# Kernel optimization log

Hardware: AMD Instinct MI355X
Metric: run time of the kernel (lower is better)

The kernel has to match this reference:

```python
import jax, jax.numpy as jnp
import numpy as np

B, S, T, V, E, H = 32, 64, 64, 32000, 256, 512


def lstm_layer(x, h0, c0, Wih, Whh, bih, bhh):
    """PyTorch-convention LSTM layer. x: [B,T,in]; gates order i,f,g,o."""
    xg = jnp.einsum('bti,gi->btg', x, Wih) + (bih + bhh)  # [B,T,4H] precomputed input gates

    def step(carry, xt):
        h, c = carry
        g = xt + h @ Whh.T
        i, f, gg, o = jnp.split(g, 4, axis=-1)
        c = jax.nn.sigmoid(f) * c + jax.nn.sigmoid(i) * jnp.tanh(gg)
        h = jax.nn.sigmoid(o) * jnp.tanh(c)
        return (h, c), h

    (hT, cT), ys = jax.lax.scan(step, (h0, c0), xg.transpose(1, 0, 2))
    return ys.transpose(1, 0, 2), hT, cT


def setup_inputs() -> dict:
    key = jax.random.key(0)
    ks = jax.random.split(key, 32)
    w = lambda k, shape: jax.random.normal(k, shape, jnp.float32) * 0.05
    return {
        'source': jax.random.randint(ks[0], (B, S), 0, V),
        'target': jax.random.randint(ks[1], (B, T), 0, V),
        'enc_emb': w(ks[2], (V, E)),
        'enc_Wih0': w(ks[3], (4 * H, E)),
        'enc_Whh0': w(ks[4], (4 * H, H)),
        'enc_bih0': w(ks[5], (4 * H,)),
        'enc_bhh0': w(ks[6], (4 * H,)),
        'enc_Wih1': w(ks[7], (4 * H, H)),
        'enc_Whh1': w(ks[8], (4 * H, H)),
        'enc_bih1': w(ks[9], (4 * H,)),
        'enc_bhh1': w(ks[10], (4 * H,)),
        'dec_emb': w(ks[11], (V, E)),
        'dec_Wih0': w(ks[12], (4 * H, E)),
        'dec_Whh0': w(ks[13], (4 * H, H)),
        'dec_bih0': w(ks[14], (4 * H,)),
        'dec_bhh0': w(ks[15], (4 * H,)),
        'dec_Wih1': w(ks[16], (4 * H, H)),
        'dec_Whh1': w(ks[17], (4 * H, H)),
        'dec_bih1': w(ks[18], (4 * H,)),
        'dec_bhh1': w(ks[19], (4 * H,)),
        'aff_W': w(ks[20], (V, H)),
        'aff_b': w(ks[21], (V,)),
    }


def reference(source, target, enc_emb, enc_Wih0, enc_Whh0, enc_bih0, enc_bhh0,
              enc_Wih1, enc_Whh1, enc_bih1, enc_bhh1, dec_emb,
              dec_Wih0, dec_Whh0, dec_bih0, dec_bhh0,
              dec_Wih1, dec_Whh1, dec_bih1, dec_bhh1, aff_W, aff_b):
    b = source.shape[0]
    z = jnp.zeros((b, H), jnp.float32)
    # Encoder: 2-layer LSTM over source, keep final (h,c) per layer
    x = enc_emb[source]                                   # [B,S,E]
    y0, h0, c0 = lstm_layer(x, z, z, enc_Wih0, enc_Whh0, enc_bih0, enc_bhh0)
    _, h1, c1 = lstm_layer(y0, z, z, enc_Wih1, enc_Whh1, enc_bih1, enc_bhh1)
    # Decoder: original loop is always teacher-forced (input = target[:, i]),
    # so it equals one full-sequence LSTM over target[:, :-1].
    dx = dec_emb[target[:, :-1]]                          # [B,T-1,E]
    d0, _, _ = lstm_layer(dx, h0, c0, dec_Wih0, dec_Whh0, dec_bih0, dec_bhh0)
    d1, _, _ = lstm_layer(d0, h1, c1, dec_Wih1, dec_Whh1, dec_bih1, dec_bhh1)
    logits = jnp.einsum('bth,vh->btv', d1, aff_W) + aff_b  # [B,T-1,V]
    # outputs[:,0,:] stays zero as in the original
    return jnp.concatenate([jnp.zeros((b, 1, logits.shape[-1]), logits.dtype), logits], axis=1)
```

## Files before the change

kernel.cpp:

```cpp
#include <hip/hip_runtime.h>
#include <hip/hip_bf16.h>

using bf16 = __hip_bfloat16;
typedef __bf16 bf16x8 __attribute__((ext_vector_type(8)));
typedef float f32x4 __attribute__((ext_vector_type(4)));
typedef int i32x4 __attribute__((ext_vector_type(4)));
typedef short short4v __attribute__((ext_vector_type(4)));
typedef short short8v __attribute__((ext_vector_type(8)));

#define DEV __device__ __forceinline__


DEV unsigned short f2bf(float f) {
  unsigned u = __builtin_bit_cast(unsigned, f);
  u = (u + 0x7fffu + ((u >> 16) & 1u)) >> 16;
  return (unsigned short)u;
}

DEV f32x4 mfma16(bf16x8 a, bf16x8 b, f32x4 c) {
  return __builtin_amdgcn_mfma_f32_16x16x32_bf16(a, b, c, 0, 0, 0);
}

DEV void llc_load16(bf16x8* dst, const bf16* p) {
  i32x4 r;
  asm volatile("global_load_dwordx4 %0, %1, off sc0 sc1" : "=v"(r) : "v"(p) : "memory");
  *dst = __builtin_bit_cast(bf16x8, r);
}
DEV void llc_store16(void* p, short8v v) {
  asm volatile("global_store_dwordx4 %0, %1, off sc0 sc1"
               :: "v"(p), "v"(__builtin_bit_cast(i32x4, v)) : "memory");
}
DEV void llc_store_f32(float* p, float v) {
  asm volatile("global_store_dword %0, %1, off sc0 sc1" :: "v"(p), "v"(v) : "memory");
}
DEV float llc_load_f32(const float* p) {
  float r;
  asm volatile("global_load_dword %0, %1, off sc0 sc1\n\ts_waitcnt vmcnt(0)"
               : "=v"(r) : "v"(p) : "memory");
  return r;
}
DEV void llc_store_flag(unsigned* p, unsigned v) {
  asm volatile("global_store_dword %0, %1, off sc0 sc1" :: "v"(p), "v"(v) : "memory");
}

DEV void poll16(const unsigned* base, int wave, int lane) {
  const unsigned* p = base + (long)(wave * 16 + (lane & 15)) * 32;
  while (true) {
    unsigned v = __hip_atomic_load(p, __ATOMIC_RELAXED, __HIP_MEMORY_SCOPE_SYSTEM);
    if (__all(v != 0u)) break;
    __builtin_amdgcn_s_sleep(1);
  }
}
DEV void poll64(const unsigned* base, int lane) {
  const unsigned* p = base + (long)lane * 32;
  while (true) {
    unsigned v = __hip_atomic_load(p, __ATOMIC_RELAXED, __HIP_MEMORY_SCOPE_SYSTEM);
    if (__all(v != 0u)) break;
    __builtin_amdgcn_s_sleep(1);
  }
}

struct ConvJobs {
  const float* src[9];
  bf16* dst[9];
  int n[9];
  int cnt;
};

__global__ void convert_all(ConvJobs jobs) {
  long base = (long)blockIdx.x * blockDim.x + threadIdx.x;
  long stride = (long)gridDim.x * blockDim.x;
  for (int ji = 0; ji < jobs.cnt; ++ji) {
    const float* s = jobs.src[ji];
    bf16* d = jobs.dst[ji];
    long n4 = (long)jobs.n[ji] >> 2;
    for (long i = base; i < n4; i += stride) {
      f32x4 v = *(const f32x4*)(s + i * 4);
      short4v o;
#pragma unroll
      for (int j = 0; j < 4; ++j) o[j] = (short)f2bf(v[j]);
      *(short4v*)((short*)d + i * 4) = o;
    }
  }
}

__global__ void embed_gather(const int* __restrict__ ids, const float* __restrict__ emb,
                             bf16* __restrict__ out, int rows, int ids_stride) {
  long total = (long)rows * 64;
  long stride = (long)gridDim.x * blockDim.x;
  for (long i = (long)blockIdx.x * blockDim.x + threadIdx.x; i < total; i += stride) {
    int row = (int)(i >> 6);
    int e = ((int)i & 63) * 4;
    int b = row & 31;
    int t = row >> 5;
    int id = ids[b * ids_stride + t];
    f32x4 v = *(const f32x4*)(emb + (long)id * 256 + e);
    short4v o;
#pragma unroll
    for (int j = 0; j < 4; ++j) o[j] = (short)f2bf(v[j]);
    *(short4v*)((short*)out + (long)row * 256 + e) = o;
  }
}

__global__ void zero_t0(float* __restrict__ out) {
  long total = 32l * 8000;
  long stride = (long)gridDim.x * blockDim.x;
  f32x4 z{};
  for (long i = (long)blockIdx.x * blockDim.x + threadIdx.x; i < total; i += stride) {
    long b = i / 8000;
    long v = i - b * 8000;
    *(f32x4*)(out + b * 64 * 32000 + v * 4) = z;
  }
}

__launch_bounds__(256)
__global__ void gemm_bf16(const bf16* __restrict__ A, const void* __restrict__ Wv, int b_fp32,
                          const float* __restrict__ bias1, const float* __restrict__ bias2,
                          float* __restrict__ C, int M, int N, int K, int affine_remap) {
  __shared__ __align__(16) bf16 As[128][64];
  __shared__ __align__(16) bf16 Bs[128][64];
  int nm = (M + 127) >> 7;
  int mt_blk = blockIdx.x % nm;
  int nt_blk = blockIdx.x / nm;
  long m0 = (long)mt_blk * 128, n0 = (long)nt_blk * 128;
  int tid = threadIdx.x;
  int lane = tid & 63, wave = tid >> 6;
  int wm = wave & 1, wn = wave >> 1;
  int fl = lane & 15, fg = lane >> 4;
  const bf16* Wb = (const bf16*)Wv;
  const float* Wf = (const float*)Wv;
  f32x4 acc[4][4] = {};

  for (int k0 = 0; k0 < K; k0 += 64) {
    __syncthreads();
#pragma unroll
    for (int i = 0; i < 4; ++i) {
      int e = (i * 256 + tid) * 8;
      int row = e >> 6;
      int col = e & 63;
      long ar = m0 + row; if (ar >= M) ar = M - 1;
      *(bf16x8*)(&As[row][col]) = *(const bf16x8*)(A + ar * (long)K + k0 + col);
      long br = n0 + row; if (br >= N) br = N - 1;
      if (b_fp32) {
        const float* p = Wf + br * (long)K + k0 + col;
        f32x4 v0 = *(const f32x4*)p;
        f32x4 v1 = *(const f32x4*)(p + 4);
        short8v o;
#pragma unroll
        for (int j = 0; j < 4; ++j) { o[j] = (short)f2bf(v0[j]); o[j + 4] = (short)f2bf(v1[j]); }
        *(short8v*)(&Bs[row][col]) = o;
      } else {
        *(bf16x8*)(&Bs[row][col]) = *(const bf16x8*)(Wb + br * (long)K + k0 + col);
      }
    }
    __syncthreads();
#pragma unroll
    for (int kt = 0; kt < 2; ++kt) {
      bf16x8 af[4], bfr[4];
#pragma unroll
      for (int x = 0; x < 4; ++x)
        af[x] = *(const bf16x8*)(&As[wm * 64 + x * 16 + fl][kt * 32 + fg * 8]);
#pragma unroll
      for (int x = 0; x < 4; ++x)
        bfr[x] = *(const bf16x8*)(&Bs[wn * 64 + x * 16 + fl][kt * 32 + fg * 8]);
#pragma unroll
      for (int mi = 0; mi < 4; ++mi)
#pragma unroll
        for (int ni = 0; ni < 4; ++ni)
          acc[mi][ni] = mfma16(af[mi], bfr[ni], acc[mi][ni]);
    }
  }
#pragma unroll
  for (int mi = 0; mi < 4; ++mi) {
#pragma unroll
    for (int ni = 0; ni < 4; ++ni) {
#pragma unroll
      for (int r = 0; r < 4; ++r) {
        long row = m0 + wm * 64 + mi * 16 + fg * 4 + r;
        long col = n0 + wn * 64 + ni * 16 + fl;
        if (row < M && col < N) {
          float v = acc[mi][ni][r];
          if (bias1) v += bias1[col];
          if (bias2) v += bias2[col];
          long orow = row;
          if (affine_remap) orow = (long)(row & 31) * 64 + (row >> 5) + 1;
          C[orow * (long)N + col] = v;
        }
      }
    }
  }
}

struct FusedParams {
  const bf16* wih[4]; const bf16* whh[4];
  const float* bih[4]; const float* bhh[4];
  const bf16* x[4];
  bf16* y[4];
  const bf16* hinit[4];
  const float* cinit[4];
  float* cfin[4];
  unsigned* flags;
};

DEV unsigned* FL(unsigned* flags, int l, int t) {
  return flags + ((long)(l * 64 + t) * 64) * 32;
}

__launch_bounds__(256)
__global__ void lstm_fused(FusedParams P) {
  __shared__ float part[4][32][33];
  __shared__ __align__(16) unsigned short h_sh[32][8];
  const int tid = threadIdx.x;
  const int lane = tid & 63, wave = tid >> 6;
  const int fl = lane & 15, fg = lane >> 4;
  const int l = blockIdx.x >> 6;
  const int slc = blockIdx.x & 63;
  const int n0 = slc * 8;
  const int b_t = tid & 31, d_t = tid >> 5;
  const int T = (l < 2) ? 64 : 63;
  const int Kx = (l & 1) ? 512 : 256;
  const int xspan = Kx >> 2;
  const int ktx = xspan >> 5;
  const bf16* __restrict__ Wih = P.wih[l];
  const bf16* __restrict__ Whh = P.whh[l];
  const bf16* __restrict__ X = P.x[l];
  bf16* __restrict__ Y = P.y[l];
  const bf16* __restrict__ Hinit = P.hinit[l];
  unsigned* flags = P.flags;

  float bsum[4];
#pragma unroll
  for (int gi = 0; gi < 4; ++gi)
    bsum[gi] = P.bih[l][gi * 512 + n0 + d_t] + P.bhh[l][gi * 512 + n0 + d_t];

  bf16x8 wfx[2][4], wfh[2][4];
#pragma unroll
  for (int nt = 0; nt < 2; ++nt) {
    int j = nt * 16 + fl;
    long row = (long)(j >> 3) * 512 + n0 + (j & 7);
#pragma unroll
    for (int kt = 0; kt < 4; ++kt) {
      if (kt < ktx)
        wfx[nt][kt] =
            *(const bf16x8*)(Wih + row * (long)Kx + wave * xspan + kt * 32 + fg * 8);
      wfh[nt][kt] = *(const bf16x8*)(Whh + row * 512l + wave * 128 + kt * 32 + fg * 8);
    }
  }
  float c = 0.f;

  for (int t = 0; t < T; ++t) {
    const unsigned* fb = (l == 1) ? FL(flags, 0, t) : (l == 3) ? FL(flags, 2, t) : nullptr;
    if (fb) poll16(fb, wave, lane);

    const bf16* xb = X + (long)t * 32 * Kx;
    bf16x8 xa0[4], xa1[4];
#pragma unroll
    for (int kt = 0; kt < 4; ++kt) {
      if (kt < ktx) {
        int k = wave * xspan + kt * 32 + fg * 8;
        const bf16* p0 = xb + (long)fl * Kx + k;
        const bf16* p1 = xb + (long)(fl + 16) * Kx + k;
        if (l & 1) {
          llc_load16(&xa0[kt], p0);
          llc_load16(&xa1[kt], p1);
        } else {
          xa0[kt] = *(const bf16x8*)p0;
          xa1[kt] = *(const bf16x8*)p1;
        }
      }
    }
    asm volatile("s_waitcnt vmcnt(0)" ::: "memory");
    __builtin_amdgcn_sched_barrier(0);
    f32x4 acc[2][2] = {};
#pragma unroll
    for (int kt = 0; kt < 4; ++kt) {
      if (kt < ktx) {
        acc[0][0] = mfma16(xa0[kt], wfx[0][kt], acc[0][0]);
        acc[0][1] = mfma16(xa0[kt], wfx[1][kt], acc[0][1]);
        acc[1][0] = mfma16(xa1[kt], wfx[0][kt], acc[1][0]);
        acc[1][1] = mfma16(xa1[kt], wfx[1][kt], acc[1][1]);
      }
    }

    if (t > 0) poll16(FL(flags, l, t - 1), wave, lane);
    else if (l == 2) poll64(FL(flags, 0, 63), lane);
    else if (l == 3) poll64(FL(flags, 1, 63), lane);
    if (t == 0) c = llc_load_f32(P.cinit[l] + (long)b_t * 512 + n0 + d_t);

    const bf16* hb = (t == 0) ? Hinit : (Y + (long)(t - 1) * 32 * 512);
    bf16x8 ha0[4], ha1[4];
#pragma unroll
    for (int kt = 0; kt < 4; ++kt) {
      int k = wave * 128 + kt * 32 + fg * 8;
      llc_load16(&ha0[kt], hb + (long)fl * 512 + k);
      llc_load16(&ha1[kt], hb + (long)(fl + 16) * 512 + k);
    }
    asm volatile("s_waitcnt vmcnt(0)" ::: "memory");
    __builtin_amdgcn_sched_barrier(0);
#pragma unroll
    for (int kt = 0; kt < 4; ++kt) {
      acc[0][0] = mfma16(ha0[kt], wfh[0][kt], acc[0][0]);
      acc[0][1] = mfma16(ha0[kt], wfh[1][kt], acc[0][1]);
      acc[1][0] = mfma16(ha1[kt], wfh[0][kt], acc[1][0]);
      acc[1][1] = mfma16(ha1[kt], wfh[1][kt], acc[1][1]);
    }
#pragma unroll
    for (int mt = 0; mt < 2; ++mt)
#pragma unroll
      for (int nt = 0; nt < 2; ++nt)
#pragma unroll
        for (int r = 0; r < 4; ++r)
          part[wave][mt * 16 + fg * 4 + r][nt * 16 + fl] = acc[mt][nt][r];
    __syncthreads();

    float g4[4];
#pragma unroll
    for (int gi = 0; gi < 4; ++gi) {
      int j = gi * 8 + d_t;
      g4[gi] = part[0][b_t][j] + part[1][b_t][j] + part[2][b_t][j] + part[3][b_t][j] +
               bsum[gi];
    }
    float ig = 1.f / (1.f + __expf(-g4[0]));
    float ff = 1.f / (1.f + __expf(-g4[1]));
    float gg = tanhf(g4[2]);
    float og = 1.f / (1.f + __expf(-g4[3]));
    c = ff * c + ig * gg;
    float h = og * tanhf(c);
    h_sh[b_t][d_t] = f2bf(h);
    if (t == T - 1) {
      llc_store_f32(P.cfin[l] + (long)b_t * 512 + n0 + d_t, c);
      asm volatile("s_waitcnt vmcnt(0)" ::: "memory");
    }
    __syncthreads();
    if (wave == 0) {
      if (lane < 32)
        llc_store16((unsigned short*)Y + ((long)t * 32 + lane) * 512 + n0,
                    *(const short8v*)(&h_sh[lane][0]));
      asm volatile("s_waitcnt vmcnt(0)" ::: "memory");
      if (lane == 0)
        llc_store_flag(FL(flags, l, t) + (long)slc * 32, 1u);
      asm volatile("s_waitcnt vmcnt(0)" ::: "memory");
    }
  }
}

extern "C" void kernel_launch(void* const* d_in, const int* in_sizes, int n_in,
                              void* d_out, int out_size, void* d_ws, size_t ws_size,
                              hipStream_t stream) {
  (void)in_sizes; (void)n_in; (void)out_size;
  const int*   source   = (const int*)d_in[0];
  const int*   target   = (const int*)d_in[1];
  const float* enc_emb  = (const float*)d_in[2];
  const float* enc_Wih0 = (const float*)d_in[3];
  const float* enc_Whh0 = (const float*)d_in[4];
  const float* enc_bih0 = (const float*)d_in[5];
  const float* enc_bhh0 = (const float*)d_in[6];
  const float* enc_Wih1 = (const float*)d_in[7];
  const float* enc_Whh1 = (const float*)d_in[8];
  const float* enc_bih1 = (const float*)d_in[9];
  const float* enc_bhh1 = (const float*)d_in[10];
  const float* dec_emb  = (const float*)d_in[11];
  const float* dec_Wih0 = (const float*)d_in[12];
  const float* dec_Whh0 = (const float*)d_in[13];
  const float* dec_bih0 = (const float*)d_in[14];
  const float* dec_bhh0 = (const float*)d_in[15];
  const float* dec_Wih1 = (const float*)d_in[16];
  const float* dec_Whh1 = (const float*)d_in[17];
  const float* dec_bih1 = (const float*)d_in[18];
  const float* dec_bhh1 = (const float*)d_in[19];
  const float* aff_W    = (const float*)d_in[20];
  const float* aff_b    = (const float*)d_in[21];
  float* out = (float*)d_out;

  size_t off = 0;
  auto alc = [&](size_t bytes) {
    char* p = (char*)d_ws + off;
    off += (bytes + 255) & ~(size_t)255;
    return (void*)p;
  };
  unsigned* FLAGS = (unsigned*)alc((size_t)4 * 64 * 64 * 32 * 4);
  bf16*  ZH  = (bf16*)alc(32 * 512 * 2);
  float* ZC  = (float*)alc(32 * 512 * 4);
  size_t zero_span = off;
  float* CE0 = (float*)alc(32 * 512 * 4);
  float* CE1 = (float*)alc(32 * 512 * 4);
  float* CD  = (float*)alc(32 * 512 * 4);
  float* CD2 = (float*)alc(32 * 512 * 4);
  bf16*  XE  = (bf16*)alc((size_t)2048 * 256 * 2);
  bf16*  XD  = (bf16*)alc((size_t)2016 * 256 * 2);
  bf16*  YE0 = (bf16*)alc((size_t)2048 * 512 * 2);
  bf16*  YE1 = (bf16*)alc((size_t)2048 * 512 * 2);
  bf16*  YD0 = (bf16*)alc((size_t)2016 * 512 * 2);
  bf16*  YD1 = (bf16*)alc((size_t)2016 * 512 * 2);
  bf16*  WI0E = (bf16*)alc((size_t)2048 * 256 * 2);
  bf16*  WH0E = (bf16*)alc((size_t)2048 * 512 * 2);
  bf16*  WI1E = (bf16*)alc((size_t)2048 * 512 * 2);
  bf16*  WH1E = (bf16*)alc((size_t)2048 * 512 * 2);
  bf16*  WI0D = (bf16*)alc((size_t)2048 * 256 * 2);
  bf16*  WH0D = (bf16*)alc((size_t)2048 * 512 * 2);
  bf16*  WI1D = (bf16*)alc((size_t)2048 * 512 * 2);
  bf16*  WH1D = (bf16*)alc((size_t)2048 * 512 * 2);
  bf16*  WAFF = (bf16*)alc((size_t)32000 * 512 * 2);
  bool use_waff = (off <= ws_size);

  hipMemsetAsync(d_ws, 0, zero_span, stream);

  ConvJobs cj;
  cj.src[0] = enc_Wih0; cj.dst[0] = WI0E; cj.n[0] = 2048 * 256;
  cj.src[1] = enc_Whh0; cj.dst[1] = WH0E; cj.n[1] = 2048 * 512;
  cj.src[2] = enc_Wih1; cj.dst[2] = WI1E; cj.n[2] = 2048 * 512;
  cj.src[3] = enc_Whh1; cj.dst[3] = WH1E; cj.n[3] = 2048 * 512;
  cj.src[4] = dec_Wih0; cj.dst[4] = WI0D; cj.n[4] = 2048 * 256;
  cj.src[5] = dec_Whh0; cj.dst[5] = WH0D; cj.n[5] = 2048 * 512;
  cj.src[6] = dec_Wih1; cj.dst[6] = WI1D; cj.n[6] = 2048 * 512;
  cj.src[7] = dec_Whh1; cj.dst[7] = WH1D; cj.n[7] = 2048 * 512;
  cj.cnt = 8;
  if (use_waff) {
    cj.src[8] = aff_W; cj.dst[8] = WAFF; cj.n[8] = 32000 * 512; cj.cnt = 9;
  }
  convert_all<<<dim3(1024), dim3(256), 0, stream>>>(cj);

  embed_gather<<<dim3(512), dim3(256), 0, stream>>>(source, enc_emb, XE, 2048, 64);
  embed_gather<<<dim3(512), dim3(256), 0, stream>>>(target, dec_emb, XD, 2016, 64);

  FusedParams P;
  P.wih[0] = WI0E; P.whh[0] = WH0E; P.bih[0] = enc_bih0; P.bhh[0] = enc_bhh0;
  P.wih[1] = WI1E; P.whh[1] = WH1E; P.bih[1] = enc_bih1; P.bhh[1] = enc_bhh1;
  P.wih[2] = WI0D; P.whh[2] = WH0D; P.bih[2] = dec_bih0; P.bhh[2] = dec_bhh0;
  P.wih[3] = WI1D; P.whh[3] = WH1D; P.bih[3] = dec_bih1; P.bhh[3] = dec_bhh1;
  P.x[0] = XE;  P.x[1] = YE0; P.x[2] = XD;  P.x[3] = YD0;
  P.y[0] = YE0; P.y[1] = YE1; P.y[2] = YD0; P.y[3] = YD1;
  P.hinit[0] = ZH; P.hinit[1] = ZH;
  P.hinit[2] = YE0 + (size_t)63 * 32 * 512;
  P.hinit[3] = YE1 + (size_t)63 * 32 * 512;
  P.cinit[0] = ZC;  P.cinit[1] = ZC;  P.cinit[2] = CE0; P.cinit[3] = CE1;
  P.cfin[0]  = CE0; P.cfin[1]  = CE1; P.cfin[2]  = CD;  P.cfin[3]  = CD2;
  P.flags = FLAGS;
  void* args[1] = {&P};
  hipLaunchCooperativeKernel((void*)lstm_fused, dim3(256), dim3(256), args, 0, stream);

  zero_t0<<<dim3(1000), dim3(256), 0, stream>>>(out);
  if (use_waff)
    gemm_bf16<<<dim3(16 * 250), dim3(256), 0, stream>>>(YD1, WAFF, 0, aff_b, nullptr,
                                                        out, 2016, 32000, 512, 1);
  else
    gemm_bf16<<<dim3(16 * 250), dim3(256), 0, stream>>>(YD1, aff_W, 1, aff_b, nullptr,
                                                        out, 2016, 32000, 512, 1);
}
```

Before: 768.4 us.

## Replace per-step flag sync with poisoned-data polling in fused LSTM kernel

Drops the separate flag array. The hidden-state and cell buffers are pre-filled with 0xFF, and consumer blocks poll the h and x slabs until no 32-bit word is all ones. Each thread now writes its bf16 h value straight to global memory. This removes the LDS staging, the store-wait-flag sequence and the extra flag round trip on every recurrent step. The costs are an extra memset of several MB and a race: two adjacent bf16 values share one polled 32-bit word, so a half-written word can pass the check.

```diff
diff --git a/kernel.cpp b/kernel.cpp
--- a/kernel.cpp
+++ b/kernel.cpp
@@ -26,36 +26,38 @@
   asm volatile("global_load_dwordx4 %0, %1, off sc0 sc1" : "=v"(r) : "v"(p) : "memory");
   *dst = __builtin_bit_cast(bf16x8, r);
 }
-DEV void llc_store16(void* p, short8v v) {
-  asm volatile("global_store_dwordx4 %0, %1, off sc0 sc1"
-               :: "v"(p), "v"(__builtin_bit_cast(i32x4, v)) : "memory");
-}
 DEV void llc_store_f32(float* p, float v) {
   asm volatile("global_store_dword %0, %1, off sc0 sc1" :: "v"(p), "v"(v) : "memory");
 }
-DEV float llc_load_f32(const float* p) {
-  float r;
-  asm volatile("global_load_dword %0, %1, off sc0 sc1\n\ts_waitcnt vmcnt(0)"
-               : "=v"(r) : "v"(p) : "memory");
-  return r;
-}
-DEV void llc_store_flag(unsigned* p, unsigned v) {
-  asm volatile("global_store_dword %0, %1, off sc0 sc1" :: "v"(p), "v"(v) : "memory");
-}
-
-DEV void poll16(const unsigned* base, int wave, int lane) {
-  const unsigned* p = base + (long)(wave * 16 + (lane & 15)) * 32;
+DEV void llc_store_u16(unsigned short* p, unsigned v) {
+  asm volatile("global_store_short %0, %1, off sc0 sc1" :: "v"(p), "v"(v) : "memory");
+}
+DEV bool valid16(bf16x8 v) {
+  i32x4 u = __builtin_bit_cast(i32x4, v);
+  return (u[0] != -1) && (u[1] != -1) && (u[2] != -1) && (u[3] != -1);
+}
+
+DEV void poll_slab(const bf16* base, int fl, int koff, bf16x8 a0[4], bf16x8 a1[4]) {
   while (true) {
-    unsigned v = __hip_atomic_load(p, __ATOMIC_RELAXED, __HIP_MEMORY_SCOPE_SYSTEM);
-    if (__all(v != 0u)) break;
+#pragma unroll
+    for (int kt = 0; kt < 4; ++kt) {
+      llc_load16(&a0[kt], base + (long)fl * 512 + koff + kt * 32);
+      llc_load16(&a1[kt], base + (long)(fl + 16) * 512 + koff + kt * 32);
+    }
+    asm volatile("s_waitcnt vmcnt(0)" ::: "memory");
+    bool ok = true;
+#pragma unroll
+    for (int kt = 0; kt < 4; ++kt) ok = ok && valid16(a0[kt]) && valid16(a1[kt]);
+    if (__all(ok)) break;
     __builtin_amdgcn_s_sleep(1);
   }
 }
-DEV void poll64(const unsigned* base, int lane) {
-  const unsigned* p = base + (long)lane * 32;
+DEV float llc_poll_f32(const float* p) {
   while (true) {
-    unsigned v = __hip_atomic_load(p, __ATOMIC_RELAXED, __HIP_MEMORY_SCOPE_SYSTEM);
-    if (__all(v != 0u)) break;
+    float r;
+    asm volatile("global_load_dword %0, %1, off sc0 sc1\n\ts_waitcnt vmcnt(0)"
+                 : "=v"(r) : "v"(p) : "memory");
+    if (__all(__builtin_bit_cast(unsigned, r) != 0xFFFFFFFFu)) return r;
     __builtin_amdgcn_s_sleep(1);
   }
 }
@@ -199,17 +201,11 @@
   const bf16* hinit[4];
   const float* cinit[4];
   float* cfin[4];
-  unsigned* flags;
 };
-
-DEV unsigned* FL(unsigned* flags, int l, int t) {
-  return flags + ((long)(l * 64 + t) * 64) * 32;
-}
 
 __launch_bounds__(256)
 __global__ void lstm_fused(FusedParams P) {
   __shared__ float part[4][32][33];
-  __shared__ __align__(16) unsigned short h_sh[32][8];
   const int tid = threadIdx.x;
   const int lane = tid & 63, wave = tid >> 6;
   const int fl = lane & 15, fg = lane >> 4;
@@ -226,7 +222,6 @@
   const bf16* __restrict__ X = P.x[l];
   bf16* __restrict__ Y = P.y[l];
   const bf16* __restrict__ Hinit = P.hinit[l];
-  unsigned* flags = P.flags;
 
   float bsum[4];
 #pragma unroll
@@ -249,54 +244,39 @@
   float c = 0.f;
 
   for (int t = 0; t < T; ++t) {
-    const unsigned* fb = (l == 1) ? FL(flags, 0, t) : (l == 3) ? FL(flags, 2, t) : nullptr;
-    if (fb) poll16(fb, wave, lane);
-
     const bf16* xb = X + (long)t * 32 * Kx;
-    bf16x8 xa0[4], xa1[4];
-#pragma unroll
-    for (int kt = 0; kt < 4; ++kt) {
-      if (kt < ktx) {
-        int k = wave * xspan + kt * 32 + fg * 8;
-        const bf16* p0 = xb + (long)fl * Kx + k;
-        const bf16* p1 = xb + (long)(fl + 16) * Kx + k;
-        if (l & 1) {
-          llc_load16(&xa0[kt], p0);
-          llc_load16(&xa1[kt], p1);
-        } else {
-          xa0[kt] = *(const bf16x8*)p0;
-          xa1[kt] = *(const bf16x8*)p1;
-        }
-      }
-    }
-    asm volatile("s_waitcnt vmcnt(0)" ::: "memory");
-    __builtin_amdgcn_sched_barrier(0);
     f32x4 acc[2][2] = {};
-#pragma unroll
-    for (int kt = 0; kt < 4; ++kt) {
-      if (kt < ktx) {
+    if (l & 1) {
+      bf16x8 xa0[4], xa1[4];
+      poll_slab(xb, fl, wave * 128 + fg * 8, xa0, xa1);
+#pragma unroll
+      for (int kt = 0; kt < 4; ++kt) {
         acc[0][0] = mfma16(xa0[kt], wfx[0][kt], acc[0][0]);
         acc[0][1] = mfma16(xa0[kt], wfx[1][kt], acc[0][1]);
         acc[1][0] = mfma16(xa1[kt], wfx[0][kt], acc[1][0]);
         acc[1][1] = mfma16(xa1[kt], wfx[1][kt], acc[1][1]);
       }
-    }
-
-    if (t > 0) poll16(FL(flags, l, t - 1), wave, lane);
-    else if (l == 2) poll64(FL(flags, 0, 63), lane);
-    else if (l == 3) poll64(FL(flags, 1, 63), lane);
-    if (t == 0) c = llc_load_f32(P.cinit[l] + (long)b_t * 512 + n0 + d_t);
+    } else {
+      bf16x8 xa0[2], xa1[2];
+#pragma unroll
+      for (int kt = 0; kt < 2; ++kt) {
+        int k = wave * xspan + kt * 32 + fg * 8;
+        xa0[kt] = *(const bf16x8*)(xb + (long)fl * Kx + k);
+        xa1[kt] = *(const bf16x8*)(xb + (long)(fl + 16) * Kx + k);
+      }
+#pragma unroll
+      for (int kt = 0; kt < 2; ++kt) {
+        acc[0][0] = mfma16(xa0[kt], wfx[0][kt], acc[0][0]);
+        acc[0][1] = mfma16(xa0[kt], wfx[1][kt], acc[0][1]);
+        acc[1][0] = mfma16(xa1[kt], wfx[0][kt], acc[1][0]);
+        acc[1][1] = mfma16(xa1[kt], wfx[1][kt], acc[1][1]);
+      }
+    }
 
     const bf16* hb = (t == 0) ? Hinit : (Y + (long)(t - 1) * 32 * 512);
     bf16x8 ha0[4], ha1[4];
-#pragma unroll
-    for (int kt = 0; kt < 4; ++kt) {
-      int k = wave * 128 + kt * 32 + fg * 8;
-      llc_load16(&ha0[kt], hb + (long)fl * 512 + k);
-      llc_load16(&ha1[kt], hb + (long)(fl + 16) * 512 + k);
-    }
-    asm volatile("s_waitcnt vmcnt(0)" ::: "memory");
-    __builtin_amdgcn_sched_barrier(0);
+    poll_slab(hb, fl, wave * 128 + fg * 8, ha0, ha1);
+    if (t == 0) c = llc_poll_f32(P.cinit[l] + (long)b_t * 512 + n0 + d_t);
 #pragma unroll
     for (int kt = 0; kt < 4; ++kt) {
       acc[0][0] = mfma16(ha0[kt], wfh[0][kt], acc[0][0]);
@@ -326,21 +306,11 @@
     float og = 1.f / (1.f + __expf(-g4[3]));
     c = ff * c + ig * gg;
     float h = og * tanhf(c);
-    h_sh[b_t][d_t] = f2bf(h);
-    if (t == T - 1) {
+    llc_store_u16((unsigned short*)Y + ((long)t * 32 + b_t) * 512 + n0 + d_t,
+                  (unsigned)f2bf(h));
+    if (t == T - 1)
       llc_store_f32(P.cfin[l] + (long)b_t * 512 + n0 + d_t, c);
-      asm volatile("s_waitcnt vmcnt(0)" ::: "memory");
-    }
     __syncthreads();
-    if (wave == 0) {
-      if (lane < 32)
-        llc_store16((unsigned short*)Y + ((long)t * 32 + lane) * 512 + n0,
-                    *(const short8v*)(&h_sh[lane][0]));
-      asm volatile("s_waitcnt vmcnt(0)" ::: "memory");
-      if (lane == 0)
-        llc_store_flag(FL(flags, l, t) + (long)slc * 32, 1u);
-      asm volatile("s_waitcnt vmcnt(0)" ::: "memory");
-    }
   }
 }
 
@@ -378,20 +348,21 @@
     off += (bytes + 255) & ~(size_t)255;
     return (void*)p;
   };
-  unsigned* FLAGS = (unsigned*)alc((size_t)4 * 64 * 64 * 32 * 4);
   bf16*  ZH  = (bf16*)alc(32 * 512 * 2);
   float* ZC  = (float*)alc(32 * 512 * 4);
   size_t zero_span = off;
+  size_t poison_begin = off;
   float* CE0 = (float*)alc(32 * 512 * 4);
   float* CE1 = (float*)alc(32 * 512 * 4);
+  bf16*  YE0 = (bf16*)alc((size_t)2048 * 512 * 2);
+  bf16*  YE1 = (bf16*)alc((size_t)2048 * 512 * 2);
+  bf16*  YD0 = (bf16*)alc((size_t)2016 * 512 * 2);
+  bf16*  YD1 = (bf16*)alc((size_t)2016 * 512 * 2);
+  size_t poison_end = off;
   float* CD  = (float*)alc(32 * 512 * 4);
   float* CD2 = (float*)alc(32 * 512 * 4);
   bf16*  XE  = (bf16*)alc((size_t)2048 * 256 * 2);
   bf16*  XD  = (bf16*)alc((size_t)2016 * 256 * 2);
-  bf16*  YE0 = (bf16*)alc((size_t)2048 * 512 * 2);
-  bf16*  YE1 = (bf16*)alc((size_t)2048 * 512 * 2);
-  bf16*  YD0 = (bf16*)alc((size_t)2016 * 512 * 2);
-  bf16*  YD1 = (bf16*)alc((size_t)2016 * 512 * 2);
   bf16*  WI0E = (bf16*)alc((size_t)2048 * 256 * 2);
   bf16*  WH0E = (bf16*)alc((size_t)2048 * 512 * 2);
   bf16*  WI1E = (bf16*)alc((size_t)2048 * 512 * 2);
@@ -404,6 +375,7 @@
   bool use_waff = (off <= ws_size);
 
   hipMemsetAsync(d_ws, 0, zero_span, stream);
+  hipMemsetAsync((char*)d_ws + poison_begin, 0xFF, poison_end - poison_begin, stream);
 
   ConvJobs cj;
   cj.src[0] = enc_Wih0; cj.dst[0] = WI0E; cj.n[0] = 2048 * 256;
@@ -435,7 +407,6 @@
   P.hinit[3] = YE1 + (size_t)63 * 32 * 512;
   P.cinit[0] = ZC;  P.cinit[1] = ZC;  P.cinit[2] = CE0; P.cinit[3] = CE1;
   P.cfin[0]  = CE0; P.cfin[1]  = CE1; P.cfin[2]  = CD;  P.cfin[3]  = CD2;
-  P.flags = FLAGS;
   void* args[1] = {&P};
   hipLaunchCooperativeKernel((void*)lstm_fused, dim3(256), dim3(256), args, 0, stream);
 
```

Measured after the change: 859.8 us. +11.9%, slower.

## Fuse output projection GEMM into persistent LSTM kernel with flag-gated tile stealing

Applied to the files above, without the earlier changes.

Appends a work-stealing GEMM loop to the cooperative LSTM kernel. Once a block finishes its recurrence, it grabs 128x128 output tiles through an atomic counter. Each tile first spins on the per-timestep flags of the last decoder layer until the rows it needs are ready. This lets idle blocks, such as the encoder-layer blocks during the decoder phase, compute logits while the recurrence is still running, and it removes the separate GEMM launch; the t0 zeroing kernel is moved before the fused launch. The tradeoff is a simple single-buffered in-kernel GEMM at only 256 blocks, with larger shared memory, and possible memory contention that slows the latency-bound recurrence.

```diff
diff --git a/kernel.cpp b/kernel.cpp
--- a/kernel.cpp
+++ b/kernel.cpp
@@ -24,6 +24,11 @@
 DEV void llc_load16(bf16x8* dst, const bf16* p) {
   i32x4 r;
   asm volatile("global_load_dwordx4 %0, %1, off sc0 sc1" : "=v"(r) : "v"(p) : "memory");
+  *dst = __builtin_bit_cast(bf16x8, r);
+}
+DEV void g_load16(bf16x8* dst, const bf16* p) {
+  i32x4 r;
+  asm volatile("global_load_dwordx4 %0, %1, off" : "=v"(r) : "v"(p) : "memory");
   *dst = __builtin_bit_cast(bf16x8, r);
 }
 DEV void llc_store16(void* p, short8v v) {
@@ -200,6 +205,11 @@
   const float* cinit[4];
   float* cfin[4];
   unsigned* flags;
+  const bf16* waff;
+  const float* affb;
+  float* out;
+  unsigned* tile_ctr;
+  int do_gemm;
 };
 
 DEV unsigned* FL(unsigned* flags, int l, int t) {
@@ -210,6 +220,9 @@
 __global__ void lstm_fused(FusedParams P) {
   __shared__ float part[4][32][33];
   __shared__ __align__(16) unsigned short h_sh[32][8];
+  __shared__ __align__(16) bf16 As[128][64];
+  __shared__ __align__(16) bf16 Bs[128][64];
+  __shared__ unsigned tile_sh;
   const int tid = threadIdx.x;
   const int lane = tid & 63, wave = tid >> 6;
   const int fl = lane & 15, fg = lane >> 4;
@@ -341,6 +354,88 @@
         llc_store_flag(FL(flags, l, t) + (long)slc * 32, 1u);
       asm volatile("s_waitcnt vmcnt(0)" ::: "memory");
     }
+  }
+
+  if (!P.do_gemm) return;
+  const bf16* Ag = P.y[3];
+  const bf16* Wg = P.waff;
+  const int wm = wave & 1, wn = wave >> 1;
+  while (true) {
+    if (tid == 0)
+      tile_sh = __hip_atomic_fetch_add(P.tile_ctr, 1u, __ATOMIC_RELAXED,
+                                       __HIP_MEMORY_SCOPE_AGENT);
+    __syncthreads();
+    unsigned tile = tile_sh;
+    if (tile >= 4000u) break;
+    int mt = tile / 250, ntb = tile - mt * 250;
+    long m0 = (long)mt * 128, gn0 = (long)ntb * 128;
+    if (wave == 0) {
+#pragma unroll
+      for (int q = 0; q < 4; ++q) {
+        int t = mt * 4 + q;
+        if (t < 63) {
+          const unsigned* f = FL(flags, 3, t) + (long)lane * 32;
+          while (__hip_atomic_load(f, __ATOMIC_RELAXED, __HIP_MEMORY_SCOPE_SYSTEM) == 0u)
+            __builtin_amdgcn_s_sleep(16);
+        }
+      }
+    }
+    __syncthreads();
+
+    f32x4 acc[4][4] = {};
+    for (int k0 = 0; k0 < 512; k0 += 64) {
+      __syncthreads();
+      bf16x8 areg[4], wreg[4];
+#pragma unroll
+      for (int i = 0; i < 4; ++i) {
+        int e = (i * 256 + tid) * 8;
+        int row = e >> 6, col = e & 63;
+        long ar = m0 + row; if (ar >= 2016) ar = 2015;
+        llc_load16(&areg[i], Ag + ar * 512 + k0 + col);
+        g_load16(&wreg[i], Wg + (gn0 + row) * 512 + k0 + col);
+      }
+      asm volatile("s_waitcnt vmcnt(0)" ::: "memory");
+#pragma unroll
+      for (int i = 0; i < 4; ++i) {
+        int e = (i * 256 + tid) * 8;
+        int row = e >> 6, col = e & 63;
+        *(bf16x8*)(&As[row][col]) = areg[i];
+        *(bf16x8*)(&Bs[row][col]) = wreg[i];
+      }
+      __syncthreads();
+#pragma unroll
+      for (int kt = 0; kt < 2; ++kt) {
+        bf16x8 af[4], bfr[4];
+#pragma unroll
+        for (int x = 0; x < 4; ++x)
+          af[x] = *(const bf16x8*)(&As[wm * 64 + x * 16 + fl][kt * 32 + fg * 8]);
+#pragma unroll
+        for (int x = 0; x < 4; ++x)
+          bfr[x] = *(const bf16x8*)(&Bs[wn * 64 + x * 16 + fl][kt * 32 + fg * 8]);
+#pragma unroll
+        for (int mi = 0; mi < 4; ++mi)
+#pragma unroll
+          for (int ni = 0; ni < 4; ++ni)
+            acc[mi][ni] = mfma16(af[mi], bfr[ni], acc[mi][ni]);
+      }
+    }
+#pragma unroll
+    for (int mi = 0; mi < 4; ++mi) {
+#pragma unroll
+      for (int ni = 0; ni < 4; ++ni) {
+#pragma unroll
+        for (int r = 0; r < 4; ++r) {
+          long row = m0 + wm * 64 + mi * 16 + fg * 4 + r;
+          long col = gn0 + wn * 64 + ni * 16 + fl;
+          if (row < 2016) {
+            float v = acc[mi][ni][r] + P.affb[col];
+            long orow = (long)(row & 31) * 64 + (row >> 5) + 1;
+            P.out[orow * 32000 + col] = v;
+          }
+        }
+      }
+    }
+    __syncthreads();
   }
 }
 
@@ -379,6 +474,7 @@
     return (void*)p;
   };
   unsigned* FLAGS = (unsigned*)alc((size_t)4 * 64 * 64 * 32 * 4);
+  unsigned* TILEC = (unsigned*)alc(256);
   bf16*  ZH  = (bf16*)alc(32 * 512 * 2);
   float* ZC  = (float*)alc(32 * 512 * 4);
   size_t zero_span = off;
@@ -422,6 +518,7 @@
 
   embed_gather<<<dim3(512), dim3(256), 0, stream>>>(source, enc_emb, XE, 2048, 64);
   embed_gather<<<dim3(512), dim3(256), 0, stream>>>(target, dec_emb, XD, 2016, 64);
+  zero_t0<<<dim3(1000), dim3(256), 0, stream>>>(out);
 
   FusedParams P;
   P.wih[0] = WI0E; P.whh[0] = WH0E; P.bih[0] = enc_bih0; P.bhh[0] = enc_bhh0;
@@ -436,14 +533,12 @@
   P.cinit[0] = ZC;  P.cinit[1] = ZC;  P.cinit[2] = CE0; P.cinit[3] = CE1;
   P.cfin[0]  = CE0; P.cfin[1]  = CE1; P.cfin[2]  = CD;  P.cfin[3]  = CD2;
   P.flags = FLAGS;
+  P.waff = WAFF; P.affb = aff_b; P.out = out; P.tile_ctr = TILEC;
+  P.do_gemm = use_waff ? 1 : 0;
   void* args[1] = {&P};
   hipLaunchCooperativeKernel((void*)lstm_fused, dim3(256), dim3(256), args, 0, stream);
 
-  zero_t0<<<dim3(1000), dim3(256), 0, stream>>>(out);
-  if (use_waff)
-    gemm_bf16<<<dim3(16 * 250), dim3(256), 0, stream>>>(YD1, WAFF, 0, aff_b, nullptr,
-                                                        out, 2016, 32000, 512, 1);
-  else
+  if (!use_waff)
     gemm_bf16<<<dim3(16 * 250), dim3(256), 0, stream>>>(YD1, aff_W, 1, aff_b, nullptr,
                                                         out, 2016, 32000, 512, 1);
 }
```

Result: faster. 744.3 us (-3.1%).
